# Performance work log

Measured on AMD Instinct MI355X. Metric: run time of the kernel, lower is better.

The kernel has to match this reference:

```python
import jax, jax.numpy as jnp
import numpy as np

D_MODEL = 1024


def pos_encoding(seq_len, d_model):
    # pos: [S,1], i: [d/2]
    pos = jnp.arange(seq_len, dtype=jnp.float32)[:, None]
    i = jnp.arange(0, d_model, 2, dtype=jnp.float32)
    angle_rates = 1.0 / jnp.power(10000.0, i / d_model)
    angle_rads = pos * angle_rates  # [S, d/2]
    # NOTE: original concatenates sin block then cos block (not interleaved)
    return jnp.concatenate([jnp.sin(angle_rads), jnp.cos(angle_rads)], axis=-1)  # [S, d]


def setup_inputs() -> dict:
    key = jax.random.key(0)
    ks = jax.random.split(key, 4)
    B, S, D = 4, 2048, D_MODEL
    scale = 1.0 / np.sqrt(D)
    x = jax.random.normal(ks[0], (B, S, D), dtype=jnp.float32)
    Wq = jax.random.normal(ks[1], (D, D), dtype=jnp.float32) * scale
    Wk = jax.random.normal(ks[2], (D, D), dtype=jnp.float32) * scale
    Wv = jax.random.normal(ks[3], (D, D), dtype=jnp.float32) * scale
    bq = jnp.zeros((D,), dtype=jnp.float32)
    bk = jnp.zeros((D,), dtype=jnp.float32)
    bv = jnp.zeros((D,), dtype=jnp.float32)
    return {"x": x, "Wq": Wq, "bq": bq, "Wk": Wk, "bk": bk, "Wv": Wv, "bv": bv}


def reference(x, Wq, bq, Wk, bk, Wv, bv):
    B, S, D = x.shape
    pe = pos_encoding(S, D)  # [S, D]
    h = x + pe[None, :, :]
    q = jnp.einsum('bsd,de->bse', h, Wq) + bq
    k = jnp.einsum('bsd,de->bse', h, Wk) + bk
    v = jnp.einsum('bsd,de->bse', h, Wv) + bv
    logits = jnp.einsum('bqd,bkd->bqk', q, k) / jnp.sqrt(jnp.float32(D))
    attn = jax.nn.softmax(logits, axis=-1)
    out = jnp.einsum('bqk,bkd->bqd', attn, v)
    return x + out
```

## Files before the change

### kernel.cpp

```cpp
#include <hip/hip_runtime.h>
#include <stdint.h>


#define AS1(p) ((__attribute__((address_space(1))) void*)(p))
#define AS3(p) ((__attribute__((address_space(3))) void*)(p))

typedef _Float16 f16x8 __attribute__((ext_vector_type(8)));
typedef _Float16 f16x4 __attribute__((ext_vector_type(4)));
typedef float f32x4 __attribute__((ext_vector_type(4)));

__global__ __launch_bounds__(256) void prep(const float* __restrict__ x,
                                            _Float16* __restrict__ h,
                                            const float* __restrict__ Wq,
                                            const float* __restrict__ Wk,
                                            const float* __restrict__ Wv,
                                            _Float16* __restrict__ Wt,
                                            float* __restrict__ rowsum) {
  const int bx = blockIdx.x;
  const int tid = threadIdx.x;
  if (bx < 8192) {
    const size_t e = ((size_t)bx * 256 + tid) * 4;
    const int d = (int)(e & 1023);
    const int s = (int)((e >> 10) & 2047);
    const float4 xv = *(const float4*)(x + e);
    const int half = d >> 9;
    const int j0 = d & 511;
    const float c = -0.017988946039016f;
    f16x4 o;
#pragma unroll
    for (int t = 0; t < 4; t++) {
      const float r = __expf((float)(j0 + t) * c);
      const float a = (float)s * r;
      const float p = half ? __cosf(a) : __sinf(a);
      const float xe = (t == 0) ? xv.x : (t == 1) ? xv.y : (t == 2) ? xv.z : xv.w;
      o[t] = (_Float16)(xe + p);
    }
    *(f16x4*)(h + e) = o;
  } else if (bx < 11264) {
    __shared__ float t[32][33];
    const int w = bx - 8192;
    const int z = w >> 10;
    const int rem = w & 1023;
    const int n0 = (rem & 31) * 32, k0 = (rem >> 5) * 32;
    const float* W = (z == 0) ? Wq : (z == 1) ? Wk : Wv;
    _Float16* o = Wt + (size_t)z * 1048576;
    const int tx = tid & 31, ty = tid >> 5;
#pragma unroll
    for (int i = ty; i < 32; i += 8)
      t[i][tx] = W[(size_t)(k0 + i) * 1024 + (n0 + tx)];
    __syncthreads();
#pragma unroll
    for (int i = ty; i < 32; i += 8)
      o[(size_t)(n0 + i) * 1024 + (k0 + tx)] = (_Float16)t[tx][i];
  } else {
    rowsum[(bx - 11264) * 256 + tid] = 0.f;
  }
}

template <int MODE>
__global__ __launch_bounds__(256) void gemm_bt(
    const _Float16* __restrict__ A0, long long sA,
    const _Float16* __restrict__ B0, long long sB,
    void* __restrict__ C0, long long sC,
    const float* __restrict__ aux0, const float* __restrict__ aux1,
    const float* __restrict__ aux2, float* __restrict__ rowsum,
    _Float16* __restrict__ vT,
    long long sX, const int K, const int N, const int ldc) {
  __shared__ __align__(16) _Float16 As[4 * 4096];
  __shared__ __align__(16) _Float16 Bs[4 * 4096];
  const int tid = threadIdx.x;
  const int bid = blockIdx.x;

  int z, bm0, bn0;
  if (MODE == 0) {
    const int c = bid & 7, t = bid >> 3;
    const int mhi = t & 7, u = t >> 3;
    bm0 = (mhi * 8 + c) * 128;
    bn0 = (u & 7) * 128;
    z = u >> 3;
  } else {
    const int c = bid & 7, t = bid >> 3;
    const int zx = (t & 3) * 8 + c;
    const int y = t >> 2;
    z = zx >> 3; bm0 = (zx & 7) * 128; bn0 = y * 128;
  }
  const _Float16* A = A0 + (size_t)z * sA;
  const _Float16* Bt = B0 + (size_t)z * sB;

  const _Float16* a0 = A + (size_t)(bm0 + (tid >> 2)) * K + (tid & 3) * 8;
  const _Float16* a1 = a0 + (size_t)64 * K;
  const _Float16* b0 = Bt + (size_t)(bn0 + (tid >> 2)) * K + (tid & 3) * 8;
  const _Float16* b1 = b0 + (size_t)64 * K;

  auto stage = [&](int s) {
    const int r = s & 3;
    const int k = s * 32;
    __builtin_amdgcn_global_load_lds(AS1(a0 + k), AS3(&As[r * 4096 + tid * 8]), 16, 0, 0);
    __builtin_amdgcn_global_load_lds(AS1(a1 + k), AS3(&As[r * 4096 + tid * 8 + 2048]), 16, 0, 0);
    __builtin_amdgcn_global_load_lds(AS1(b0 + k), AS3(&Bs[r * 4096 + tid * 8]), 16, 0, 0);
    __builtin_amdgcn_global_load_lds(AS1(b1 + k), AS3(&Bs[r * 4096 + tid * 8 + 2048]), 16, 0, 0);
  };

  const int lane = tid & 63, wave = tid >> 6;
  const int wr = wave >> 1, wc = wave & 1;
  const int quad = lane >> 4, l16 = lane & 15;

  f32x4 acc[4][4];
#pragma unroll
  for (int i = 0; i < 4; i++)
#pragma unroll
    for (int j = 0; j < 4; j++) {
      f32x4 zz = {0.f, 0.f, 0.f, 0.f};
      acc[i][j] = zz;
    }

  const int NS = K >> 5;

  stage(0); stage(1); stage(2);
  asm volatile("s_waitcnt vmcnt(8)" ::: "memory");
  __builtin_amdgcn_s_barrier();

  for (int s = 0; s < NS; ++s) {
    const int r = s & 3;
    f16x8 af[4], bf[4];
#pragma unroll
    for (int i = 0; i < 4; i++)
      af[i] = *(const f16x8*)&As[r * 4096 + (wr * 64 + i * 16 + l16) * 32 + quad * 8];
#pragma unroll
    for (int j = 0; j < 4; j++)
      bf[j] = *(const f16x8*)&Bs[r * 4096 + (wc * 64 + j * 16 + l16) * 32 + quad * 8];
    if (s + 3 < NS) stage(s + 3);
    __builtin_amdgcn_s_barrier();
    asm volatile("s_waitcnt lgkmcnt(0)" ::: "memory");
    __builtin_amdgcn_sched_barrier(0);
    __builtin_amdgcn_s_setprio(1);
#pragma unroll
    for (int i = 0; i < 4; i++)
#pragma unroll
      for (int j = 0; j < 4; j++)
        acc[i][j] = __builtin_amdgcn_mfma_f32_16x16x32_f16(af[i], bf[j],
                                                           acc[i][j], 0, 0, 0);
    __builtin_amdgcn_s_setprio(0);
    __builtin_amdgcn_sched_barrier(0);
    if (s + 1 < NS) {
      if (s + 3 < NS)       asm volatile("s_waitcnt vmcnt(8)" ::: "memory");
      else if (s + 3 == NS) asm volatile("s_waitcnt vmcnt(4)" ::: "memory");
      else                  asm volatile("s_waitcnt vmcnt(0)" ::: "memory");
      __builtin_amdgcn_s_barrier();
    }
  }

  const int rowb = bm0 + wr * 64 + quad * 4;
  const int colb = bn0 + wc * 64 + l16;
  if (MODE == 0) {
    const float* bias = (z == 0) ? aux0 : (z == 1) ? aux1 : aux2;
    if (z == 2) {
      const int b = rowb >> 11, sl = rowb & 2047;
      _Float16* vb = vT + (size_t)b * 2097152;
#pragma unroll
      for (int i = 0; i < 4; i++)
#pragma unroll
        for (int j = 0; j < 4; j++) {
          const int gn = colb + j * 16;
          const float bb = bias[gn];
          f16x4 o;
#pragma unroll
          for (int r = 0; r < 4; r++) o[r] = (_Float16)(acc[i][j][r] + bb);
          *(f16x4*)&vb[(size_t)gn * 2048 + sl + i * 16] = o;
        }
    } else {
      _Float16* C = (_Float16*)C0 + (size_t)z * sC;
#pragma unroll
      for (int i = 0; i < 4; i++)
#pragma unroll
        for (int j = 0; j < 4; j++) {
          const int gn = colb + j * 16;
          const float bb = bias[gn];
#pragma unroll
          for (int r = 0; r < 4; r++)
            C[(size_t)(rowb + i * 16 + r) * N + gn] = (_Float16)(acc[i][j][r] + bb);
        }
    }
  } else {
    float* C = (float*)C0 + (size_t)z * sC;
    const float* X = aux0 + (size_t)z * sX;
    float inv[4];
#pragma unroll
    for (int j = 0; j < 4; j++)
      inv[j] = 1.0f / rowsum[z * 2048 + colb + j * 16];
#pragma unroll
    for (int i = 0; i < 4; i++)
#pragma unroll
      for (int j = 0; j < 4; j++) {
        const int gn = colb + j * 16;
        const size_t base = (size_t)gn * ldc + rowb + i * 16;
        const float4 xv = *(const float4*)(X + base);
        float4 o;
        o.x = acc[i][j][0] * inv[j] + xv.x;
        o.y = acc[i][j][1] * inv[j] + xv.y;
        o.z = acc[i][j][2] * inv[j] + xv.z;
        o.w = acc[i][j][3] * inv[j] + xv.w;
        *(float4*)(C + base) = o;
      }
  }
}

#define RD_A(SET, S_)                                                         \
  {                                                                           \
    _Pragma("unroll") for (int fi = 0; fi < 4; fi++)                          \
      _Pragma("unroll") for (int kk = 0; kk < 2; kk++)                        \
        SET[fi * 2 + kk] = *(const f16x8*)&As[bb][kk][                        \
            (wr * 128 + (S_) * 64 + fi * 16 + l16) * 32 + quad * 8];          \
  }
#define RD_B(SET, S_)                                                         \
  {                                                                           \
    _Pragma("unroll") for (int fj = 0; fj < 2; fj++)                          \
      _Pragma("unroll") for (int kk = 0; kk < 2; kk++)                        \
        SET[fj * 2 + kk] = *(const f16x8*)&Bs[bb][kk][                        \
            (wc * 64 + (S_) * 32 + fj * 16 + l16) * 32 + quad * 8];           \
  }
#define MFMA16(ASET, BSET, MQ, NQ)                                            \
  {                                                                           \
    __builtin_amdgcn_s_setprio(1);                                            \
    _Pragma("unroll") for (int fi = 0; fi < 4; fi++)                          \
      _Pragma("unroll") for (int fj = 0; fj < 2; fj++)                        \
        _Pragma("unroll") for (int kk = 0; kk < 2; kk++)                      \
          acc[(MQ) * 4 + fi][(NQ) * 2 + fj] =                                 \
              __builtin_amdgcn_mfma_f32_16x16x32_f16(                         \
                  ASET[fi * 2 + kk], BSET[fj * 2 + kk],                       \
                  acc[(MQ) * 4 + fi][(NQ) * 2 + fj], 0, 0, 0);                \
    __builtin_amdgcn_s_setprio(0);                                            \
  }
#define PHASE_WAIT()                                                          \
  __builtin_amdgcn_s_barrier();                                               \
  asm volatile("s_waitcnt lgkmcnt(0)" ::: "memory");                          \
  __builtin_amdgcn_sched_barrier(0);

__global__ __launch_bounds__(512) void gemm256_logits(
    const _Float16* __restrict__ A0, long long sA,
    const _Float16* __restrict__ B0, long long sB,
    void* __restrict__ C0, long long sC,
    float* __restrict__ rowsum, const int K, const int ldc) {
  __shared__ __align__(16) _Float16 As[2][2][8192];
  __shared__ __align__(16) _Float16 Bs[2][2][8192];
  const int tid = threadIdx.x;
  const int bid = blockIdx.x;

  const int w = (bid & 7) * 32 + (bid >> 3);
  const int z = w >> 6;
  const int r0 = w & 63;
  const int bm0 = (r0 >> 3) * 256, bn0 = (r0 & 7) * 256;

  const _Float16* A = A0 + (size_t)z * sA;
  const _Float16* Bt = B0 + (size_t)z * sB;

  const _Float16* aS = A + (size_t)(bm0 + (tid >> 2)) * K + (tid & 3) * 8;
  const _Float16* bS = Bt + (size_t)(bn0 + (tid >> 2)) * K + (tid & 3) * 8;
  const size_t halfStep = (size_t)128 * K;

  auto stageA = [&](int X, int h) {
    const int b = X & 1;
    const _Float16* s = aS + (size_t)X * 64 + (size_t)h * halfStep;
    _Float16* d = &As[b][0][h * 4096 + tid * 8];
    __builtin_amdgcn_global_load_lds(AS1(s), AS3(d), 16, 0, 0);
    __builtin_amdgcn_global_load_lds(AS1(s + 32), AS3(d + 8192), 16, 0, 0);
  };
  auto stageB = [&](int X, int h) {
    const int b = X & 1;
    const _Float16* s = bS + (size_t)X * 64 + (size_t)h * halfStep;
    _Float16* d = &Bs[b][0][h * 4096 + tid * 8];
    __builtin_amdgcn_global_load_lds(AS1(s), AS3(d), 16, 0, 0);
    __builtin_amdgcn_global_load_lds(AS1(s + 32), AS3(d + 8192), 16, 0, 0);
  };

  const int lane = tid & 63, wave = tid >> 6;
  const int wr = wave >> 2, wc = wave & 3;
  const int quad = lane >> 4, l16 = lane & 15;

  f32x4 acc[8][4];
#pragma unroll
  for (int i = 0; i < 8; i++)
#pragma unroll
    for (int j = 0; j < 4; j++) {
      f32x4 zz = {0.f, 0.f, 0.f, 0.f};
      acc[i][j] = zz;
    }

  const int nt = K >> 6;

  stageA(0, 0); stageA(0, 1); stageB(0, 0); stageB(0, 1);
  stageA(1, 0); stageA(1, 1);
  asm volatile("s_waitcnt vmcnt(4)" ::: "memory");
  __builtin_amdgcn_s_barrier();

  f16x8 a0[8], a1[8], b0f[4], b1f[4];

  for (int T = 0; T < nt; ++T) {
    const int bb = T & 1;
    RD_A(a0, 0);
    RD_B(b0f, 0);
    if (T + 1 < nt) stageB(T + 1, 0);
    PHASE_WAIT();
    MFMA16(a0, b0f, 0, 0);
    __builtin_amdgcn_s_barrier();
    RD_A(a1, 1);
    if (T + 1 < nt) stageB(T + 1, 1);
    PHASE_WAIT();
    MFMA16(a1, b0f, 1, 0);
    __builtin_amdgcn_s_barrier();
    RD_B(b1f, 1);
    if (T + 2 < nt) stageA(T + 2, 0);
    PHASE_WAIT();
    MFMA16(a0, b1f, 0, 1);
    __builtin_amdgcn_s_barrier();
    if (T + 2 < nt) stageA(T + 2, 1);
    PHASE_WAIT();
    MFMA16(a1, b1f, 1, 1);
    if (T + 1 < nt) {
      if (T + 2 < nt) asm volatile("s_waitcnt vmcnt(4)" ::: "memory");
      else            asm volatile("s_waitcnt vmcnt(0)" ::: "memory");
      __builtin_amdgcn_s_barrier();
    }
  }

  const int rowb = bm0 + wr * 128 + quad * 4;
  const int colb = bn0 + wc * 64 + l16;
  _Float16* C = (_Float16*)C0 + (size_t)z * sC;
  float rs[4] = {0.f, 0.f, 0.f, 0.f};
#pragma unroll
  for (int i = 0; i < 8; i++)
#pragma unroll
    for (int j = 0; j < 4; j++) {
      const int gn = colb + j * 16;
      f16x4 o;
      float pj = 0.f;
#pragma unroll
      for (int r = 0; r < 4; r++) {
        const float e = __expf(acc[i][j][r] * 0.03125f);
        o[r] = (_Float16)e;
        pj += e;
      }
      rs[j] += pj;
      *(f16x4*)&C[(size_t)gn * ldc + rowb + i * 16] = o;
    }
#pragma unroll
  for (int j = 0; j < 4; j++) {
    float v = rs[j];
    v += __shfl_xor(v, 16);
    v += __shfl_xor(v, 32);
    if (quad == 0) atomicAdd(&rowsum[z * 2048 + colb + j * 16], v);
  }
}

extern "C" void kernel_launch(void* const* d_in, const int* in_sizes, int n_in,
                              void* d_out, int out_size, void* d_ws, size_t ws_size,
                              hipStream_t stream) {
  (void)in_sizes; (void)n_in; (void)out_size; (void)ws_size;
  const float* x  = (const float*)d_in[0];
  const float* Wq = (const float*)d_in[1];
  const float* bq = (const float*)d_in[2];
  const float* Wk = (const float*)d_in[3];
  const float* bk = (const float*)d_in[4];
  const float* Wv = (const float*)d_in[5];
  const float* bv = (const float*)d_in[6];
  float* out = (float*)d_out;
  char* ws = (char*)d_ws;

  _Float16* h    = (_Float16*)(ws);
  _Float16* Wt   = (_Float16*)(ws + 16777216);
  _Float16* qkv  = (_Float16*)(ws + 23068672);
  _Float16* attn = (_Float16*)(ws + 73400320);
  float* rowsum  = (float*)   (ws + 106954752);

  const long long E = 8388608;
  _Float16* vT = qkv + 2 * E;

  prep<<<11296, 256, 0, stream>>>(x, h, Wq, Wk, Wv, Wt, rowsum);

  gemm_bt<0><<<1536, 256, 0, stream>>>(
      h, 0LL, Wt, 1048576LL, qkv, E, bq, bk, bv, nullptr, vT,
      0LL, 1024, 1024, 0);

  gemm256_logits<<<256, 512, 0, stream>>>(
      qkv + E, 2097152LL, qkv, 2097152LL, attn, 4194304LL,
      rowsum, 1024, 2048);

  gemm_bt<2><<<512, 256, 0, stream>>>(
      vT, 2097152LL, attn, 4194304LL, out, 2097152LL,
      x, nullptr, nullptr, rowsum, nullptr,
      2097152LL, 2048, 2048, 1024);
}
```

Measured before the change: 259.6 us.

## Use three-stage LDS ring with one barrier per K-step in GEMM

Shrinks the GEMM's global-to-LDS prefetch ring from four buffers to three, using rotating offsets instead of s&3 indexing. The prefetch for step s+2 is now issued before the LDS fragment reads. The mid-iteration barrier, the lgkmcnt wait and the sched_barriers are removed, so each K-step synchronises once. This is meant to cut barrier overhead, let the compiler overlap LDS reads with MFMAs, and lower LDS use so more blocks can be resident per CU. The cost is a shallower prefetch depth, which may expose more global-memory latency.

```diff
diff --git a/kernel.cpp b/kernel.cpp
--- a/kernel.cpp
+++ b/kernel.cpp
@@ -66,8 +66,8 @@
     const float* __restrict__ aux2, float* __restrict__ rowsum,
     _Float16* __restrict__ vT,
     long long sX, const int K, const int N, const int ldc) {
-  __shared__ __align__(16) _Float16 As[4 * 4096];
-  __shared__ __align__(16) _Float16 Bs[4 * 4096];
+  __shared__ __align__(16) _Float16 As[3 * 4096];
+  __shared__ __align__(16) _Float16 Bs[3 * 4096];
   const int tid = threadIdx.x;
   const int bid = blockIdx.x;
 
@@ -92,13 +92,12 @@
   const _Float16* b0 = Bt + (size_t)(bn0 + (tid >> 2)) * K + (tid & 3) * 8;
   const _Float16* b1 = b0 + (size_t)64 * K;
 
-  auto stage = [&](int s) {
-    const int r = s & 3;
-    const int k = s * 32;
-    __builtin_amdgcn_global_load_lds(AS1(a0 + k), AS3(&As[r * 4096 + tid * 8]), 16, 0, 0);
-    __builtin_amdgcn_global_load_lds(AS1(a1 + k), AS3(&As[r * 4096 + tid * 8 + 2048]), 16, 0, 0);
-    __builtin_amdgcn_global_load_lds(AS1(b0 + k), AS3(&Bs[r * 4096 + tid * 8]), 16, 0, 0);
-    __builtin_amdgcn_global_load_lds(AS1(b1 + k), AS3(&Bs[r * 4096 + tid * 8 + 2048]), 16, 0, 0);
+  auto stage = [&](int kt, int rbase) {
+    const int k = kt * 32;
+    __builtin_amdgcn_global_load_lds(AS1(a0 + k), AS3(&As[rbase + tid * 8]), 16, 0, 0);
+    __builtin_amdgcn_global_load_lds(AS1(a1 + k), AS3(&As[rbase + tid * 8 + 2048]), 16, 0, 0);
+    __builtin_amdgcn_global_load_lds(AS1(b0 + k), AS3(&Bs[rbase + tid * 8]), 16, 0, 0);
+    __builtin_amdgcn_global_load_lds(AS1(b1 + k), AS3(&Bs[rbase + tid * 8 + 2048]), 16, 0, 0);
   };
 
   const int lane = tid & 63, wave = tid >> 6;
@@ -116,23 +115,21 @@
 
   const int NS = K >> 5;
 
-  stage(0); stage(1); stage(2);
-  asm volatile("s_waitcnt vmcnt(8)" ::: "memory");
+  stage(0, 0); stage(1, 4096);
+  asm volatile("s_waitcnt vmcnt(4)" ::: "memory");
   __builtin_amdgcn_s_barrier();
 
+  int rb = 0;
+  int sb = 8192;
   for (int s = 0; s < NS; ++s) {
-    const int r = s & 3;
+    if (s + 2 < NS) stage(s + 2, sb);
     f16x8 af[4], bf[4];
 #pragma unroll
     for (int i = 0; i < 4; i++)
-      af[i] = *(const f16x8*)&As[r * 4096 + (wr * 64 + i * 16 + l16) * 32 + quad * 8];
+      af[i] = *(const f16x8*)&As[rb + (wr * 64 + i * 16 + l16) * 32 + quad * 8];
 #pragma unroll
     for (int j = 0; j < 4; j++)
-      bf[j] = *(const f16x8*)&Bs[r * 4096 + (wc * 64 + j * 16 + l16) * 32 + quad * 8];
-    if (s + 3 < NS) stage(s + 3);
-    __builtin_amdgcn_s_barrier();
-    asm volatile("s_waitcnt lgkmcnt(0)" ::: "memory");
-    __builtin_amdgcn_sched_barrier(0);
+      bf[j] = *(const f16x8*)&Bs[rb + (wc * 64 + j * 16 + l16) * 32 + quad * 8];
     __builtin_amdgcn_s_setprio(1);
 #pragma unroll
     for (int i = 0; i < 4; i++)
@@ -141,13 +138,13 @@
         acc[i][j] = __builtin_amdgcn_mfma_f32_16x16x32_f16(af[i], bf[j],
                                                            acc[i][j], 0, 0, 0);
     __builtin_amdgcn_s_setprio(0);
-    __builtin_amdgcn_sched_barrier(0);
     if (s + 1 < NS) {
-      if (s + 3 < NS)       asm volatile("s_waitcnt vmcnt(8)" ::: "memory");
-      else if (s + 3 == NS) asm volatile("s_waitcnt vmcnt(4)" ::: "memory");
-      else                  asm volatile("s_waitcnt vmcnt(0)" ::: "memory");
+      if (s + 2 < NS) asm volatile("s_waitcnt vmcnt(4)" ::: "memory");
+      else            asm volatile("s_waitcnt vmcnt(0)" ::: "memory");
       __builtin_amdgcn_s_barrier();
     }
+    rb = (rb == 8192) ? 0 : rb + 4096;
+    sb = (sb == 8192) ? 0 : sb + 4096;
   }
 
   const int rowb = bm0 + wr * 64 + quad * 4;
```

After: 264.1 us. No clear change (+1.7%).
